# Optimization experiments

Hardware: AMD Instinct MI355X
Metric: run time of the kernel (lower is better)

## Reference

```python
import jax, jax.numpy as jnp
import numpy as np

B, IN, H, DK, E = 16, 1024, 1024, 1024, 4
D1 = DK * E  # 4096
LR = 0.01


def _xavier(key, shape):
    fan_out, fan_in = shape
    bound = float(np.sqrt(6.0 / (fan_in + fan_out)))
    return jax.random.uniform(key, shape, jnp.float32, -bound, bound)


def setup_inputs() -> dict:
    key = jax.random.key(0)
    ks = jax.random.split(key, 6)
    return {
        "x_t": jax.random.normal(ks[0], (B, IN), jnp.float32),
        "W_k": _xavier(ks[1], (DK, IN)),   # key_proj.weight
        "W_v": _xavier(ks[2], (H, IN)),    # value_proj.weight
        "W_o": _xavier(ks[3], (IN, H)),    # output_proj.weight
        "W0": _xavier(ks[4], (D1, DK)),    # memory_mlp[0].weight
        "W1": _xavier(ks[5], (H, D1)),     # memory_mlp[2].weight
    }


def reference(x_t, W_k, W_v, W_o, W0, W1):
    # projections
    k_t = x_t @ W_k.T  # [B, DK]
    v_t = x_t @ W_v.T  # [B, H]

    def step(k, v):
        # fast-weight MLP forward + per-sample TTT-style gradient update
        def loss_fn(params):
            W0_, W1_ = params
            h = W1_ @ jax.nn.gelu(W0_ @ k, approximate=False)  # [H]
            loss = 0.5 * jnp.mean((h - v) ** 2)  # F.mse_loss mean over H
            return loss, h

        (_, h), (gW0, gW1) = jax.value_and_grad(loss_fn, has_aux=True)((W0, W1))
        return h, W0 - LR * gW0, W1 - LR * gW1

    hidden, W0_new, W1_new = jax.vmap(step)(k_t, v_t)  # [B,H], [B,D1,DK], [B,H,D1]
    output = hidden @ W_o.T  # [B, IN]
    return output, W0_new, W1_new
```

## Files before the change

kernel.cpp:

```cpp
#include <hip/hip_runtime.h>
#include <hip/hip_bf16.h>
#include <math.h>

#define B_   16
#define IN_  1024
#define H_   1024
#define DK_  1024
#define D1_  4096
#define LR_  0.01f

typedef float vf4 __attribute__((ext_vector_type(4)));

#define ROWGEMM_BODY(WPTR, VPTR, K)                                         \
  __shared__ float vtile[16][256];                                          \
  const int tid  = threadIdx.x;                                             \
  const int wave = tid >> 6;                                                \
  const int lane = tid & 63;                                                \
  float acc[16];                                                            \
  _Pragma("unroll")                                                         \
  for (int b = 0; b < 16; ++b) acc[b] = 0.f;                                \
  for (int k0 = 0; k0 < (K); k0 += 256) {                                   \
    __syncthreads();                                                        \
    _Pragma("unroll")                                                       \
    for (int idx = tid; idx < 1024; idx += 256) {                           \
      int bb = idx >> 6;                                                    \
      int cc = (idx & 63) << 2;                                             \
      *(vf4*)&vtile[bb][cc] = *(const vf4*)((VPTR) + (size_t)bb * (K) + k0 + cc); \
    }                                                                       \
    __syncthreads();                                                        \
    const int c = lane << 2;                                                \
    vf4 w4 = *(const vf4*)((WPTR) + k0 + c);                                \
    _Pragma("unroll")                                                       \
    for (int b = 0; b < 16; ++b) {                                          \
      vf4 v4 = *(const vf4*)&vtile[b][c];                                   \
      acc[b] += w4.x * v4.x + w4.y * v4.y + w4.z * v4.z + w4.w * v4.w;      \
    }                                                                       \
  }                                                                         \
  _Pragma("unroll")                                                         \
  for (int b = 0; b < 16; ++b) {                                            \
    float a = acc[b];                                                       \
    _Pragma("unroll")                                                       \
    for (int off = 32; off; off >>= 1) a += __shfl_down(a, off, 64);        \
    acc[b] = a;                                                             \
  }

__global__ __launch_bounds__(256) void rowgemm16(
    const float* __restrict__ W, const float* __restrict__ V,
    float* __restrict__ out, int R, int K) {
  const int row = blockIdx.x * 4 + (threadIdx.x >> 6);
  const float* wrow = W + (size_t)row * K;
  ROWGEMM_BODY(wrow, V, K)
  if (lane == 0) {
#pragma unroll
    for (int b = 0; b < 16; ++b) out[(size_t)b * R + row] = acc[b];
  }
}

__global__ __launch_bounds__(256) void proj_kernel(
    const float* __restrict__ W_k, const float* __restrict__ W_v,
    const float* __restrict__ x, float* __restrict__ kt, float* __restrict__ vt) {
  const int grow = blockIdx.x * 4 + (threadIdx.x >> 6);
  const int row  = grow & 1023;
  const float* wrow = (grow < 1024 ? W_k : W_v) + (size_t)row * 1024;
  float* out = (grow < 1024) ? kt : vt;
  ROWGEMM_BODY(wrow, x, 1024)
  if (lane == 0) {
#pragma unroll
    for (int b = 0; b < 16; ++b) out[b * 1024 + row] = acc[b];
  }
}

__global__ __launch_bounds__(256) void z_gelu_kernel(
    const float* __restrict__ W0, const float* __restrict__ kt,
    float* __restrict__ g, float* __restrict__ gp) {
  const int row = blockIdx.x * 4 + (threadIdx.x >> 6);
  const float* wrow = W0 + (size_t)row * 1024;
  ROWGEMM_BODY(wrow, kt, 1024)
  if (lane == 0) {
#pragma unroll
    for (int b = 0; b < 16; ++b) {
      const float x   = acc[b];
      const float cdf = 0.5f * (1.f + erff(x * 0.70710678118654752f));
      g[b * 4096 + row]  = x * cdf;
      gp[b * 4096 + row] = cdf + x * 0.39894228040143268f * expf(-0.5f * x * x);
    }
  }
}

__global__ __launch_bounds__(256) void h_dh_kernel(
    const float* __restrict__ W1, const float* __restrict__ g,
    const float* __restrict__ vt, float* __restrict__ h, float* __restrict__ dh) {
  const int row = blockIdx.x * 4 + (threadIdx.x >> 6);
  const float* wrow = W1 + (size_t)row * 4096;
  ROWGEMM_BODY(wrow, g, 4096)
  if (lane == 0) {
#pragma unroll
    for (int b = 0; b < 16; ++b) {
      const float hv = acc[b];
      h[b * 1024 + row]  = hv;
      dh[b * 1024 + row] = (hv - vt[b * 1024 + row]) * (1.0f / 1024.0f);
    }
  }
}

__global__ __launch_bounds__(256) void colgemm_partial(
    const float* __restrict__ W1, const float* __restrict__ dh,
    float* __restrict__ partial) {
  __shared__ float dhs[16][64];
  const int t  = threadIdx.x;
  const int j  = blockIdx.x * 256 + t;
  const int i0 = blockIdx.y * 64;
#pragma unroll
  for (int idx = t; idx < 16 * 64; idx += 256) {
    int b = idx >> 6, c = idx & 63;
    dhs[b][c] = dh[b * 1024 + i0 + c];
  }
  __syncthreads();
  float acc[16];
#pragma unroll
  for (int b = 0; b < 16; ++b) acc[b] = 0.f;
  for (int c = 0; c < 64; ++c) {
    float w = W1[(size_t)(i0 + c) * D1_ + j];
#pragma unroll
    for (int b = 0; b < 16; ++b) acc[b] += w * dhs[b][c];
  }
  const int s = blockIdx.y;
#pragma unroll
  for (int b = 0; b < 16; ++b)
    partial[((size_t)s * 16 + b) * D1_ + j] = acc[b];
}

__global__ __launch_bounds__(256) void reduce_dz(
    const float* __restrict__ partial, const float* __restrict__ gp,
    float* __restrict__ dz) {
  const int idx = blockIdx.x * 256 + threadIdx.x;
  float s = 0.f;
#pragma unroll
  for (int p = 0; p < 16; ++p) s += partial[(size_t)p * (16 * D1_) + idx];
  dz[idx] = s * gp[idx];
}

__global__ __launch_bounds__(256) void update_both(
    const float* __restrict__ W0, const float* __restrict__ dz,
    const float* __restrict__ kt,
    const float* __restrict__ W1, const float* __restrict__ dh,
    const float* __restrict__ g,
    float* __restrict__ out1, float* __restrict__ out2) {
  const int t   = threadIdx.x;
  const int blk = blockIdx.x;
  if (blk < 1024) {
    const int i0 = blk << 2;
    const int j  = t << 2;
    vf4 w[4];
#pragma unroll
    for (int r = 0; r < 4; ++r)
      w[r] = *(const vf4*)(W0 + ((size_t)(i0 + r) << 10) + j);
#pragma unroll
    for (int b = 0; b < 16; ++b) {
      const vf4 k4 = *(const vf4*)(kt + (b << 10) + j);
      float* ob = out1 + ((size_t)b << 22);
#pragma unroll
      for (int r = 0; r < 4; ++r) {
        const float d = LR_ * dz[(b << 12) + i0 + r];
        *(vf4*)(ob + ((size_t)(i0 + r) << 10) + j) = w[r] - d * k4;
      }
    }
  } else {
    const int i = blk - 1024;
    vf4 w[4];
#pragma unroll
    for (int c = 0; c < 4; ++c)
      w[c] = *(const vf4*)(W1 + ((size_t)i << 12) + (c << 10) + (t << 2));
#pragma unroll
    for (int b = 0; b < 16; ++b) {
      const float d = LR_ * dh[(b << 10) + i];
      float* ob = out2 + ((size_t)b << 22) + ((size_t)i << 12);
      const float* gb = g + (b << 12);
#pragma unroll
      for (int c = 0; c < 4; ++c) {
        const vf4 g4 = *(const vf4*)(gb + (c << 10) + (t << 2));
        *(vf4*)(ob + (c << 10) + (t << 2)) = w[c] - d * g4;
      }
    }
  }
}

extern "C" void kernel_launch(void* const* d_in, const int* in_sizes, int n_in,
                              void* d_out, int out_size, void* d_ws, size_t ws_size,
                              hipStream_t stream) {
  const float* x_t = (const float*)d_in[0];
  const float* W_k = (const float*)d_in[1];
  const float* W_v = (const float*)d_in[2];
  const float* W_o = (const float*)d_in[3];
  const float* W0  = (const float*)d_in[4];
  const float* W1  = (const float*)d_in[5];

  float* out0 = (float*)d_out;
  float* out1 = out0 + 16384;
  float* out2 = out1 + (size_t)16 * 4096 * 1024;

  float* ws      = (float*)d_ws;
  float* kt      = ws;
  float* vt      = kt + 16384;
  float* z       = vt + 16384;
  float* g       = z + 65536;
  float* gp      = g + 65536;
  float* h       = gp + 65536;
  float* dh      = h + 16384;
  float* dz      = dh + 16384;
  float* partial = dz + 65536;

  proj_kernel<<<512, 256, 0, stream>>>(W_k, W_v, x_t, kt, vt);
  z_gelu_kernel<<<1024, 256, 0, stream>>>(W0, kt, g, gp);
  h_dh_kernel<<<256, 256, 0, stream>>>(W1, g, vt, h, dh);
  colgemm_partial<<<dim3(16, 16), 256, 0, stream>>>(W1, dh, partial);
  reduce_dz<<<256, 256, 0, stream>>>(partial, gp, dz);
  rowgemm16<<<256, 256, 0, stream>>>(W_o, h, out0, 1024, 1024);
  update_both<<<2048, 256, 0, stream>>>(W0, dz, kt, W1, dh, g, out1, out2);
}
```

Before: 650.4 us.

## Fuse dz reduction and output projection into the weight-update kernel

Removes the separate reduce_dz and rowgemm16 launches. Each W0-update block now reduces its own 4 rows of dz from the 16 partials with 16-lane shuffles into shared memory. The output projection GEMM runs as extra blocks appended to the update grid. This saves two kernel launches and the dz round trip through global memory, at the cost of each block re-reading partials and a mixed-role grid.

```diff
diff --git a/kernel.cpp b/kernel.cpp
--- a/kernel.cpp
+++ b/kernel.cpp
@@ -14,7 +14,6 @@
 #define ROWGEMM_BODY(WPTR, VPTR, K)                                         \
   __shared__ float vtile[16][256];                                          \
   const int tid  = threadIdx.x;                                             \
-  const int wave = tid >> 6;                                                \
   const int lane = tid & 63;                                                \
   float acc[16];                                                            \
   _Pragma("unroll")                                                         \
@@ -40,21 +39,9 @@
   for (int b = 0; b < 16; ++b) {                                            \
     float a = acc[b];                                                       \
     _Pragma("unroll")                                                       \
-    for (int off = 32; off; off >>= 1) a += __shfl_down(a, off, 64);        \
+    for (int m = 32; m; m >>= 1) a += __shfl_xor(a, m, 64);                 \
     acc[b] = a;                                                             \
   }
-
-__global__ __launch_bounds__(256) void rowgemm16(
-    const float* __restrict__ W, const float* __restrict__ V,
-    float* __restrict__ out, int R, int K) {
-  const int row = blockIdx.x * 4 + (threadIdx.x >> 6);
-  const float* wrow = W + (size_t)row * K;
-  ROWGEMM_BODY(wrow, V, K)
-  if (lane == 0) {
-#pragma unroll
-    for (int b = 0; b < 16; ++b) out[(size_t)b * R + row] = acc[b];
-  }
-}
 
 __global__ __launch_bounds__(256) void proj_kernel(
     const float* __restrict__ W_k, const float* __restrict__ W_v,
@@ -130,27 +117,31 @@
     partial[((size_t)s * 16 + b) * D1_ + j] = acc[b];
 }
 
-__global__ __launch_bounds__(256) void reduce_dz(
-    const float* __restrict__ partial, const float* __restrict__ gp,
-    float* __restrict__ dz) {
-  const int idx = blockIdx.x * 256 + threadIdx.x;
-  float s = 0.f;
-#pragma unroll
-  for (int p = 0; p < 16; ++p) s += partial[(size_t)p * (16 * D1_) + idx];
-  dz[idx] = s * gp[idx];
-}
-
-__global__ __launch_bounds__(256) void update_both(
-    const float* __restrict__ W0, const float* __restrict__ dz,
-    const float* __restrict__ kt,
+__global__ __launch_bounds__(256) void mega_kernel(
+    const float* __restrict__ W0, const float* __restrict__ partial,
+    const float* __restrict__ gp, const float* __restrict__ kt,
     const float* __restrict__ W1, const float* __restrict__ dh,
     const float* __restrict__ g,
-    float* __restrict__ out1, float* __restrict__ out2) {
+    const float* __restrict__ W_o, const float* __restrict__ h,
+    float* __restrict__ out0, float* __restrict__ out1, float* __restrict__ out2) {
+  const int blk = blockIdx.x;
   const int t   = threadIdx.x;
-  const int blk = blockIdx.x;
   if (blk < 1024) {
+    __shared__ float dzs[16][4];
     const int i0 = blk << 2;
-    const int j  = t << 2;
+    {
+      const int b = t >> 4;
+      const int s = t & 15;
+#pragma unroll
+      for (int r = 0; r < 4; ++r) {
+        float p = partial[(size_t)(s * 16 + b) * 4096 + i0 + r];
+#pragma unroll
+        for (int m = 8; m; m >>= 1) p += __shfl_xor(p, m, 16);
+        if (s == 0) dzs[b][r] = p * gp[(b << 12) + i0 + r];
+      }
+    }
+    __syncthreads();
+    const int j = t << 2;
     vf4 w[4];
 #pragma unroll
     for (int r = 0; r < 4; ++r)
@@ -161,11 +152,11 @@
       float* ob = out1 + ((size_t)b << 22);
 #pragma unroll
       for (int r = 0; r < 4; ++r) {
-        const float d = LR_ * dz[(b << 12) + i0 + r];
+        const float d = LR_ * dzs[b][r];
         *(vf4*)(ob + ((size_t)(i0 + r) << 10) + j) = w[r] - d * k4;
       }
     }
-  } else {
+  } else if (blk < 2048) {
     const int i = blk - 1024;
     vf4 w[4];
 #pragma unroll
@@ -181,6 +172,14 @@
         const vf4 g4 = *(const vf4*)(gb + (c << 10) + (t << 2));
         *(vf4*)(ob + (c << 10) + (t << 2)) = w[c] - d * g4;
       }
+    }
+  } else {
+    const int row = (blk - 2048) * 4 + (t >> 6);
+    const float* wrow = W_o + (size_t)row * 1024;
+    ROWGEMM_BODY(wrow, h, 1024)
+    if (lane == 0) {
+#pragma unroll
+      for (int b = 0; b < 16; ++b) out0[b * 1024 + row] = acc[b];
     }
   }
 }
@@ -202,19 +201,17 @@
   float* ws      = (float*)d_ws;
   float* kt      = ws;
   float* vt      = kt + 16384;
-  float* z       = vt + 16384;
-  float* g       = z + 65536;
+  float* g       = vt + 16384;
   float* gp      = g + 65536;
   float* h       = gp + 65536;
   float* dh      = h + 16384;
-  float* dz      = dh + 16384;
-  float* partial = dz + 65536;
+  float* partial = dh + 16384;
 
   proj_kernel<<<512, 256, 0, stream>>>(W_k, W_v, x_t, kt, vt);
   z_gelu_kernel<<<1024, 256, 0, stream>>>(W0, kt, g, gp);
   h_dh_kernel<<<256, 256, 0, stream>>>(W1, g, vt, h, dh);
   colgemm_partial<<<dim3(16, 16), 256, 0, stream>>>(W1, dh, partial);
-  reduce_dz<<<256, 256, 0, stream>>>(partial, gp, dz);
-  rowgemm16<<<256, 256, 0, stream>>>(W_o, h, out0, 1024, 1024);
-  update_both<<<2048, 256, 0, stream>>>(W0, dz, kt, W1, dh, g, out1, out2);
-}
+  mega_kernel<<<2304, 256, 0, stream>>>(W0, partial, gp, kt,
+                                        W1, dh, g, W_o, h,
+                                        out0, out1, out2);
+}
```

New measurement: 655.7 us. About the same (+0.8%).
